# Performance work log

Hardware: AMD Instinct MI355X
Metric: run time of the kernel (lower is better)

Reference implementation:

```python
import jax, jax.numpy as jnp
import numpy as np

B, C, H, W = 2, 256, 64, 64
NUM_HEADS = 4
HEAD_DIM = C // NUM_HEADS
N = H * W


def setup_inputs() -> dict:
    key = jax.random.key(0)
    ks = jax.random.split(key, 10)
    x = jax.random.normal(ks[0], (B, C, H, W), dtype=jnp.float32)
    # mostly-True mask; diagonal forced True so every row has a valid key
    m = jax.random.uniform(ks[1], (B, N, N)) > 0.1
    spatial_mask = m | jnp.eye(N, dtype=bool)[None]
    s = 1.0 / np.sqrt(C)
    wq = jax.random.normal(ks[2], (C, C), dtype=jnp.float32) * s
    bq = jnp.zeros((C,), jnp.float32)
    wk = jax.random.normal(ks[3], (C, C), dtype=jnp.float32) * s
    bk = jnp.zeros((C,), jnp.float32)
    wv = jax.random.normal(ks[4], (C, C), dtype=jnp.float32) * s
    bv = jnp.zeros((C,), jnp.float32)
    # torch zero-inits out_proj; use random weights for a non-trivial baseline
    wo = jax.random.normal(ks[5], (C, C), dtype=jnp.float32) * s
    bo = jnp.zeros((C,), jnp.float32)
    return {"x": x, "spatial_mask": spatial_mask, "wq": wq, "bq": bq,
            "wk": wk, "bk": bk, "wv": wv, "bv": bv, "wo": wo, "bo": bo}


def reference(x, spatial_mask, wq, bq, wk, bk, wv, bv, wo, bo):
    b, c, h, w = x.shape
    n = h * w
    nh, hd = NUM_HEADS, HEAD_DIM
    scale = hd ** -0.5
    x_flat = x.reshape(b, c, n).transpose(0, 2, 1)           # [b, n, c]
    q = (x_flat @ wq.T + bq).reshape(b, n, nh, hd).transpose(0, 2, 1, 3)
    k = (x_flat @ wk.T + bk).reshape(b, n, nh, hd).transpose(0, 2, 1, 3)
    v = (x_flat @ wv.T + bv).reshape(b, n, nh, hd).transpose(0, 2, 1, 3)
    logits = jnp.einsum('bhqd,bhkd->bhqk', q, k) * scale      # [b, nh, n, n]
    logits = jnp.where(spatial_mask[:, None], logits, -jnp.inf)
    attn = jax.nn.softmax(logits, axis=-1)                    # dropout = identity (eval)
    out = jnp.einsum('bhqk,bhkd->bhqd', attn, v)              # [b, nh, n, hd]
    out = out.transpose(0, 2, 1, 3).reshape(b, n, c)
    out = out @ wo.T + bo
    return out.transpose(0, 2, 1).reshape(b, c, h, w)
```

## Files before the change

### kernel.cpp

```cpp
#include <hip/hip_runtime.h>
#include <math.h>

namespace {
constexpr int B_    = 2;
constexpr int C_    = 256;
constexpr int NHEAD = 4;
constexpr int HDIM  = 64;
constexpr int NTOK  = 4096;
constexpr float SCALE = 0.125f;
constexpr float LOG2E = 1.44269504f;
}

typedef _Float16 half8  __attribute__((ext_vector_type(8)));
typedef _Float16 half4  __attribute__((ext_vector_type(4)));
typedef float    floatx4 __attribute__((ext_vector_type(4)));

__global__ __launch_bounds__(256) void pack_mask(
    const unsigned int* __restrict__ m32, unsigned int* __restrict__ packed)
{
    int c0 = 0, c1 = 0, c2 = 0, c3 = 0;
    #pragma unroll
    for (int i = 0; i < 16; i++) {
        const unsigned int d = m32[i];
        c0 += (d == 0x00000001u);
        c1 += (d == 0x3F803F80u);
        c2 += (d == 0x3F800000u);
        c3 += (d == 0x01010101u);
    }
    int fmt = 1, best = c1;
    if (c0 > best) { best = c0; fmt = 0; }
    if (c2 > best) { best = c2; fmt = 2; }
    if (c3 > best) { best = c3; fmt = 3; }

    const unsigned int W = blockIdx.x * 256 + threadIdx.x;
    unsigned int bits = 0;
    if (fmt == 1) {
        const uint4* p4 = (const uint4*)(m32 + (size_t)W * 16);
        #pragma unroll
        for (int i = 0; i < 4; i++) {
            const uint4 v = p4[i];
            const unsigned int d[4] = { v.x, v.y, v.z, v.w };
            #pragma unroll
            for (int j = 0; j < 4; j++) {
                const int e = i * 8 + j * 2;
                bits |= ((d[j] & 0xFFFFu) ? 1u : 0u) << e;
                bits |= ((d[j] >> 16)     ? 1u : 0u) << (e + 1);
            }
        }
    } else if (fmt != 3) {
        const uint4* p4 = (const uint4*)(m32 + (size_t)W * 32);
        #pragma unroll
        for (int i = 0; i < 8; i++) {
            const uint4 v = p4[i];
            bits |= (v.x ? 1u : 0u) << (i * 4 + 0);
            bits |= (v.y ? 1u : 0u) << (i * 4 + 1);
            bits |= (v.z ? 1u : 0u) << (i * 4 + 2);
            bits |= (v.w ? 1u : 0u) << (i * 4 + 3);
        }
    } else {
        const uint4* p4 = (const uint4*)(m32 + (size_t)W * 8);
        #pragma unroll
        for (int i = 0; i < 2; i++) {
            const uint4 v = p4[i];
            const unsigned int d[4] = { v.x, v.y, v.z, v.w };
            #pragma unroll
            for (int j = 0; j < 4; j++) {
                const int e = (i * 4 + j) * 4;
                bits |= ((d[j] & 0x000000FFu) ? 1u : 0u) << (e + 0);
                bits |= ((d[j] & 0x0000FF00u) ? 1u : 0u) << (e + 1);
                bits |= ((d[j] & 0x00FF0000u) ? 1u : 0u) << (e + 2);
                bits |= ((d[j] & 0xFF000000u) ? 1u : 0u) << (e + 3);
            }
        }
    }
    packed[W] = bits;
}

__global__ __launch_bounds__(256) void qkv_mfma(
    const float* __restrict__ x,
    const float* __restrict__ wq, const float* __restrict__ bq,
    const float* __restrict__ wk, const float* __restrict__ bk,
    const float* __restrict__ wv, const float* __restrict__ bv,
    _Float16* __restrict__ qo, _Float16* __restrict__ ko,
    _Float16* __restrict__ vo)
{
    const int nt = blockIdx.x;
    const int h  = blockIdx.y;
    const int b  = blockIdx.z / 3;
    const int p  = blockIdx.z % 3;

    const float* w; const float* bias;
    if (p == 0)      { w = wq; bias = bq; }
    else if (p == 1) { w = wk; bias = bk; }
    else             { w = wv; bias = bv; }

    const int t    = threadIdx.x;
    const int wid  = t >> 6;
    const int lane = t & 63;
    const int quad = lane >> 4;
    const int l15  = lane & 15;
    const int n0  = nt * 64;
    const int co0 = h * 64;

    __shared__ _Float16 wsh[64 * 72];
    __shared__ _Float16 xsh[64 * 72];
    __shared__ _Float16 tbuf[64 * 72];

    const int srow = t >> 2;
    const int sc   = (t & 3) * 16;
    const int cr   = t >> 4;
    const int nu   = (t & 15) * 4;

    floatx4 acc[4];
    #pragma unroll
    for (int i = 0; i < 4; i++) acc[i] = (floatx4)0.f;

    const float* xb = x + (size_t)b * C_ * NTOK;

    for (int c0 = 0; c0 < C_; c0 += 64) {
        {
            const float* wr = &w[(size_t)(co0 + srow) * C_ + c0 + sc];
            half8 h0, h1;
            #pragma unroll
            for (int u = 0; u < 2; u++) {
                const float4 a = *(const float4*)&wr[u * 4];
                h0[u*4+0]=(_Float16)a.x; h0[u*4+1]=(_Float16)a.y;
                h0[u*4+2]=(_Float16)a.z; h0[u*4+3]=(_Float16)a.w;
            }
            #pragma unroll
            for (int u = 0; u < 2; u++) {
                const float4 a = *(const float4*)&wr[8 + u * 4];
                h1[u*4+0]=(_Float16)a.x; h1[u*4+1]=(_Float16)a.y;
                h1[u*4+2]=(_Float16)a.z; h1[u*4+3]=(_Float16)a.w;
            }
            *(half8*)&wsh[srow * 72 + sc]     = h0;
            *(half8*)&wsh[srow * 72 + sc + 8] = h1;
        }
        {
            #pragma unroll
            for (int pass = 0; pass < 4; pass++) {
                const int cl = pass * 16 + cr;
                const float4 v = *(const float4*)&xb[(size_t)(c0 + cl) * NTOK + n0 + nu];
                xsh[(nu + 0) * 72 + cl] = (_Float16)v.x;
                xsh[(nu + 1) * 72 + cl] = (_Float16)v.y;
                xsh[(nu + 2) * 72 + cl] = (_Float16)v.z;
                xsh[(nu + 3) * 72 + cl] = (_Float16)v.w;
            }
        }
        __syncthreads();
        const half8 a0 = *(const half8*)&wsh[(wid * 16 + l15) * 72 + quad * 8];
        const half8 a1 = *(const half8*)&wsh[(wid * 16 + l15) * 72 + 32 + quad * 8];
        #pragma unroll
        for (int nt2 = 0; nt2 < 4; nt2++) {
            const half8 b0 = *(const half8*)&xsh[(nt2 * 16 + l15) * 72 + quad * 8];
            const half8 b1 = *(const half8*)&xsh[(nt2 * 16 + l15) * 72 + 32 + quad * 8];
            acc[nt2] = __builtin_amdgcn_mfma_f32_16x16x32_f16(a0, b0, acc[nt2], 0, 0, 0);
            acc[nt2] = __builtin_amdgcn_mfma_f32_16x16x32_f16(a1, b1, acc[nt2], 0, 0, 0);
        }
        __syncthreads();
    }

    const float4 bb4 = *(const float4*)&bias[co0 + wid * 16 + quad * 4];
    const float bb[4] = { bb4.x, bb4.y, bb4.z, bb4.w };

    if (p < 2) {
        const float osc = (p == 0) ? (SCALE * LOG2E) : 1.0f;
        #pragma unroll
        for (int nt2 = 0; nt2 < 4; nt2++) {
            half4 hv;
            #pragma unroll
            for (int i = 0; i < 4; i++)
                hv[i] = (_Float16)((acc[nt2][i] + bb[i]) * osc);
            *(half4*)&tbuf[(nt2 * 16 + l15) * 72 + wid * 16 + quad * 4] = hv;
        }
        __syncthreads();
        _Float16* dh = (p == 0 ? qo : ko) + (size_t)(b * NHEAD + h) * NTOK * HDIM;
        const half8 o0 = *(const half8*)&tbuf[srow * 72 + sc];
        const half8 o1 = *(const half8*)&tbuf[srow * 72 + sc + 8];
        *(half8*)&dh[(size_t)(n0 + srow) * HDIM + sc]     = o0;
        *(half8*)&dh[(size_t)(n0 + srow) * HDIM + sc + 8] = o1;
    } else {
        #pragma unroll
        for (int nt2 = 0; nt2 < 4; nt2++)
            #pragma unroll
            for (int i = 0; i < 4; i++)
                tbuf[(wid * 16 + quad * 4 + i) * 72 + nt2 * 16 + l15] =
                    (_Float16)(acc[nt2][i] + bb[i]);
        __syncthreads();
        _Float16* vth = vo + (size_t)(b * NHEAD + h) * HDIM * NTOK;
        const half8 o0 = *(const half8*)&tbuf[srow * 72 + sc];
        const half8 o1 = *(const half8*)&tbuf[srow * 72 + sc + 8];
        *(half8*)&vth[(size_t)srow * NTOK + n0 + sc]     = o0;
        *(half8*)&vth[(size_t)srow * NTOK + n0 + sc + 8] = o1;
    }
}

__global__ __launch_bounds__(512) void attn(
    const _Float16* __restrict__ q, const _Float16* __restrict__ k,
    const _Float16* __restrict__ vt, const unsigned int* __restrict__ mpacked,
    _Float16* __restrict__ ao)
{
    const int b  = blockIdx.z;
    const int h  = blockIdx.y;
    const int q0 = blockIdx.x * 64;
    const int t    = threadIdx.x;
    const int w    = t >> 6;
    const int lane = t & 63;
    const int quad = lane >> 4;
    const int l15  = lane & 15;
    const int half = w >> 2;
    const int w4   = w & 3;
    const int koff = half * (NTOK / 2);

    __shared__ __align__(16) _Float16 ksA[64 * 72];
    __shared__ __align__(16) _Float16 vsA[64 * 72];
    __shared__ __align__(16) _Float16 psA[64 * 72];
    __shared__ __align__(16) _Float16 ksB[64 * 72];
    __shared__ __align__(16) _Float16 vsB[64 * 72];
    __shared__ __align__(16) _Float16 psB[64 * 72];

    _Float16* ksc = half ? ksB : ksA;
    _Float16* vsc = half ? vsB : vsA;
    _Float16* ps  = half ? psB : psA;

    const size_t head_off = (size_t)(b * NHEAD + h) * NTOK * HDIM;
    const _Float16* qb  = q  + head_off;
    const _Float16* kb  = k  + head_off;
    const _Float16* vtb = vt + head_off;
    const unsigned int* mrow = mpacked + (size_t)b * NTOK * 128;

    const int qrow = q0 + w4 * 16 + l15;
    half8 aq0 = *(const half8*)&qb[(size_t)qrow * HDIM + quad * 8];
    half8 aq1 = *(const half8*)&qb[(size_t)qrow * HDIM + 32 + quad * 8];
    const unsigned int* mq = &mrow[(size_t)qrow * 128];

    const int tl   = t & 255;
    const int srow = tl >> 2;
    const int scol = (tl & 3) * 16;

    half8 kreg0 = *(const half8*)&kb[(size_t)(koff + srow) * HDIM + scol];
    half8 kreg1 = *(const half8*)&kb[(size_t)(koff + srow) * HDIM + scol + 8];
    half8 vreg0 = *(const half8*)&vtb[(size_t)srow * NTOK + koff + scol];
    half8 vreg1 = *(const half8*)&vtb[(size_t)srow * NTOK + koff + scol + 8];

    float l_loc = 0.f;
    floatx4 o_acc[4];
    #pragma unroll
    for (int i = 0; i < 4; i++) o_acc[i] = (floatx4)0.f;

    for (int kt = 0; kt < NTOK / 128; kt++) {
        const int k0 = koff + kt * 64;
        __syncthreads();
        *(half8*)&ksc[srow * 72 + scol]     = kreg0;
        *(half8*)&ksc[srow * 72 + scol + 8] = kreg1;
        *(half8*)&vsc[srow * 72 + scol]     = vreg0;
        *(half8*)&vsc[srow * 72 + scol + 8] = vreg1;
        __syncthreads();

        if (kt + 1 < NTOK / 128) {
            kreg0 = *(const half8*)&kb[(size_t)(k0 + 64 + srow) * HDIM + scol];
            kreg1 = *(const half8*)&kb[(size_t)(k0 + 64 + srow) * HDIM + scol + 8];
            vreg0 = *(const half8*)&vtb[(size_t)srow * NTOK + k0 + 64 + scol];
            vreg1 = *(const half8*)&vtb[(size_t)srow * NTOK + k0 + 64 + scol + 8];
        }
        const uint2 mw = *(const uint2*)&mq[k0 >> 5];

        floatx4 sa[4];
        #pragma unroll
        for (int ct = 0; ct < 4; ct++) {
            sa[ct] = (floatx4)0.f;
            const half8 ka0 = *(const half8*)&ksc[(ct * 16 + l15) * 72 + quad * 8];
            const half8 ka1 = *(const half8*)&ksc[(ct * 16 + l15) * 72 + 32 + quad * 8];
            sa[ct] = __builtin_amdgcn_mfma_f32_16x16x32_f16(ka0, aq0, sa[ct], 0, 0, 0);
            sa[ct] = __builtin_amdgcn_mfma_f32_16x16x32_f16(ka1, aq1, sa[ct], 0, 0, 0);
        }

        #pragma unroll
        for (int ct = 0; ct < 4; ct++) {
            const unsigned int word = (ct < 2) ? mw.x : mw.y;
            const unsigned nib = (word >> (((ct & 1) << 4) + quad * 4)) & 0xFu;
            half4 pv;
            #pragma unroll
            for (int i = 0; i < 4; i++) {
                const float v = ((nib >> i) & 1u) ? sa[ct][i] : -3.0e38f;
                const float p = exp2f(fminf(v, 15.f));
                l_loc += p;
                pv[i] = (_Float16)p;
            }
            *(half4*)&ps[(w4 * 16 + l15) * 72 + ct * 16 + quad * 4] = pv;
        }

        const half8 pb0 = *(const half8*)&ps[(w4 * 16 + l15) * 72 + quad * 8];
        const half8 pb1 = *(const half8*)&ps[(w4 * 16 + l15) * 72 + 32 + quad * 8];
        #pragma unroll
        for (int dt = 0; dt < 4; dt++) {
            const half8 va0 = *(const half8*)&vsc[(dt * 16 + l15) * 72 + quad * 8];
            const half8 va1 = *(const half8*)&vsc[(dt * 16 + l15) * 72 + 32 + quad * 8];
            o_acc[dt] = __builtin_amdgcn_mfma_f32_16x16x32_f16(va0, pb0, o_acc[dt], 0, 0, 0);
            o_acc[dt] = __builtin_amdgcn_mfma_f32_16x16x32_f16(va1, pb1, o_acc[dt], 0, 0, 0);
        }
    }

    l_loc += __shfl_xor(l_loc, 16, 64);
    l_loc += __shfl_xor(l_loc, 32, 64);

    __syncthreads();
    float* oex = (float*)ksA;
    float* lex = (float*)vsA;
    if (w >= 4) {
        float* dst = &oex[((size_t)(w - 4) * 64 + lane) * 16];
        #pragma unroll
        for (int dt = 0; dt < 4; dt++)
            *(floatx4*)&dst[dt * 4] = o_acc[dt];
        if (quad == 0) lex[(w - 4) * 16 + l15] = l_loc;
    }
    __syncthreads();
    if (w < 4) {
        const float* src = &oex[((size_t)w * 64 + lane) * 16];
        const float lt = l_loc + lex[w * 16 + l15];
        const float inv = (lt > 0.f) ? (1.0f / lt) : 0.f;
        _Float16* aob = ao + ((size_t)b * NTOK + q0 + w * 16 + l15) * C_ + h * 64;
        #pragma unroll
        for (int dt = 0; dt < 4; dt++) {
            const floatx4 o2 = *(const floatx4*)&src[dt * 4];
            half4 r;
            #pragma unroll
            for (int rr = 0; rr < 4; rr++)
                r[rr] = (_Float16)((o_acc[dt][rr] + o2[rr]) * inv);
            *(half4*)&aob[dt * 16 + quad * 4] = r;
        }
    }
}

__global__ __launch_bounds__(256) void out_mfma(
    const _Float16* __restrict__ ao, const float* __restrict__ wo,
    const float* __restrict__ bo, float* __restrict__ out)
{
    const int nt  = blockIdx.x;
    const int cot = blockIdx.y;
    const int b   = blockIdx.z;
    const int t    = threadIdx.x;
    const int wid  = t >> 6;
    const int lane = t & 63;
    const int quad = lane >> 4;
    const int l15  = lane & 15;
    const int n0  = nt * 64;
    const int co0 = cot * 64;

    __shared__ _Float16 wsh[64 * 72];
    __shared__ _Float16 ash[64 * 72];
    __shared__ float    tf[64 * 68];

    const int srow = t >> 2;
    const int sc   = (t & 3) * 16;

    floatx4 acc[4];
    #pragma unroll
    for (int i = 0; i < 4; i++) acc[i] = (floatx4)0.f;

    const _Float16* aob = ao + ((size_t)b * NTOK + n0) * C_;

    for (int c0 = 0; c0 < C_; c0 += 64) {
        {
            const float* wr = &wo[(size_t)(co0 + srow) * C_ + c0 + sc];
            half8 h0, h1;
            #pragma unroll
            for (int u = 0; u < 2; u++) {
                const float4 a = *(const float4*)&wr[u * 4];
                h0[u*4+0]=(_Float16)a.x; h0[u*4+1]=(_Float16)a.y;
                h0[u*4+2]=(_Float16)a.z; h0[u*4+3]=(_Float16)a.w;
            }
            #pragma unroll
            for (int u = 0; u < 2; u++) {
                const float4 a = *(const float4*)&wr[8 + u * 4];
                h1[u*4+0]=(_Float16)a.x; h1[u*4+1]=(_Float16)a.y;
                h1[u*4+2]=(_Float16)a.z; h1[u*4+3]=(_Float16)a.w;
            }
            *(half8*)&wsh[srow * 72 + sc]     = h0;
            *(half8*)&wsh[srow * 72 + sc + 8] = h1;
        }
        {
            const _Float16* ar = &aob[(size_t)srow * C_ + c0 + sc];
            *(half8*)&ash[srow * 72 + sc]     = *(const half8*)&ar[0];
            *(half8*)&ash[srow * 72 + sc + 8] = *(const half8*)&ar[8];
        }
        __syncthreads();
        const half8 a0 = *(const half8*)&wsh[(wid * 16 + l15) * 72 + quad * 8];
        const half8 a1 = *(const half8*)&wsh[(wid * 16 + l15) * 72 + 32 + quad * 8];
        #pragma unroll
        for (int nt2 = 0; nt2 < 4; nt2++) {
            const half8 b0 = *(const half8*)&ash[(nt2 * 16 + l15) * 72 + quad * 8];
            const half8 b1 = *(const half8*)&ash[(nt2 * 16 + l15) * 72 + 32 + quad * 8];
            acc[nt2] = __builtin_amdgcn_mfma_f32_16x16x32_f16(a0, b0, acc[nt2], 0, 0, 0);
            acc[nt2] = __builtin_amdgcn_mfma_f32_16x16x32_f16(a1, b1, acc[nt2], 0, 0, 0);
        }
        __syncthreads();
    }

    #pragma unroll
    for (int nt2 = 0; nt2 < 4; nt2++)
        #pragma unroll
        for (int i = 0; i < 4; i++)
            tf[(wid * 16 + quad * 4 + i) * 68 + nt2 * 16 + l15] = acc[nt2][i];
    __syncthreads();

    const int row = t >> 2;
    const int c4  = (t & 3) * 16;
    const float bb = bo[co0 + row];
    float* orow = &out[((size_t)(b * C_ + co0 + row)) * NTOK + n0 + c4];
    #pragma unroll
    for (int u = 0; u < 4; u++) {
        float4 v = *(const float4*)&tf[row * 68 + c4 + u * 4];
        v.x += bb; v.y += bb; v.z += bb; v.w += bb;
        *(float4*)&orow[u * 4] = v;
    }
}

extern "C" void kernel_launch(void* const* d_in, const int* in_sizes, int n_in,
                              void* d_out, int out_size, void* d_ws, size_t ws_size,
                              hipStream_t stream) {
    const float* x    = (const float*)d_in[0];
    const void*  mask = d_in[1];
    const float* wq   = (const float*)d_in[2];
    const float* bq   = (const float*)d_in[3];
    const float* wk   = (const float*)d_in[4];
    const float* bk   = (const float*)d_in[5];
    const float* wv   = (const float*)d_in[6];
    const float* bv   = (const float*)d_in[7];
    const float* wo   = (const float*)d_in[8];
    const float* bo   = (const float*)d_in[9];
    float* out = (float*)d_out;

    const size_t qkv_elems = (size_t)B_ * NHEAD * NTOK * HDIM;
    _Float16* wsh = (_Float16*)d_ws;
    _Float16* qbuf  = wsh;
    _Float16* kbuf  = wsh + qkv_elems;
    _Float16* vtbuf = wsh + 2 * qkv_elems;
    _Float16* aobuf = wsh + 3 * qkv_elems;
    unsigned int* mpacked = (unsigned int*)(wsh + 4 * qkv_elems);

    pack_mask<<<dim3((B_ * NTOK * 128) / 256), 256, 0, stream>>>(
        (const unsigned int*)mask, mpacked);
    qkv_mfma<<<dim3(NTOK / 64, NHEAD, B_ * 3), 256, 0, stream>>>(
        x, wq, bq, wk, bk, wv, bv, qbuf, kbuf, vtbuf);
    attn<<<dim3(NTOK / 64, NHEAD, B_), 512, 0, stream>>>(
        qbuf, kbuf, vtbuf, mpacked, aobuf);
    out_mfma<<<dim3(NTOK / 64, C_ / 64, B_), 256, 0, stream>>>(
        aobuf, wo, bo, out);
}
```

Measured before the change: 318.3 us.

## Stage full x tile once per block across heads; cheapen softmax exp/convert

The QKV projection kernel now loads and converts the whole 64-token by 256-channel x tile into shared memory once, then loops over all four heads inside the block. This replaces the earlier design of one block per head, which re-read x once per head. The grid shrinks to 4x fewer blocks, which lowers parallelism, and shared memory use per block grows. In the attention kernel, the masked exp2 now uses the hardware builtin without the fminf clamp, and the fp16 conversion uses packed round-toward-zero. That removes some ALU work but drops the overflow guard and changes the rounding mode.

```diff
diff --git a/kernel.cpp b/kernel.cpp
--- a/kernel.cpp
+++ b/kernel.cpp
@@ -13,6 +13,7 @@
 
 typedef _Float16 half8  __attribute__((ext_vector_type(8)));
 typedef _Float16 half4  __attribute__((ext_vector_type(4)));
+typedef __fp16   fp16x2 __attribute__((ext_vector_type(2)));
 typedef float    floatx4 __attribute__((ext_vector_type(4)));
 
 __global__ __launch_bounds__(256) void pack_mask(
@@ -85,9 +86,8 @@
     _Float16* __restrict__ vo)
 {
     const int nt = blockIdx.x;
-    const int h  = blockIdx.y;
-    const int b  = blockIdx.z / 3;
-    const int p  = blockIdx.z % 3;
+    const int b  = blockIdx.y;
+    const int p  = blockIdx.z;
 
     const float* w; const float* bias;
     if (p == 0)      { w = wq; bias = bq; }
@@ -99,99 +99,102 @@
     const int lane = t & 63;
     const int quad = lane >> 4;
     const int l15  = lane & 15;
-    const int n0  = nt * 64;
-    const int co0 = h * 64;
-
+    const int n0   = nt * 64;
+
+    __shared__ _Float16 xsh[64 * 264];
     __shared__ _Float16 wsh[64 * 72];
-    __shared__ _Float16 xsh[64 * 72];
     __shared__ _Float16 tbuf[64 * 72];
 
     const int srow = t >> 2;
     const int sc   = (t & 3) * 16;
-    const int cr   = t >> 4;
-    const int nu   = (t & 15) * 4;
-
-    floatx4 acc[4];
-    #pragma unroll
-    for (int i = 0; i < 4; i++) acc[i] = (floatx4)0.f;
-
-    const float* xb = x + (size_t)b * C_ * NTOK;
-
-    for (int c0 = 0; c0 < C_; c0 += 64) {
-        {
-            const float* wr = &w[(size_t)(co0 + srow) * C_ + c0 + sc];
-            half8 h0, h1;
-            #pragma unroll
-            for (int u = 0; u < 2; u++) {
-                const float4 a = *(const float4*)&wr[u * 4];
-                h0[u*4+0]=(_Float16)a.x; h0[u*4+1]=(_Float16)a.y;
-                h0[u*4+2]=(_Float16)a.z; h0[u*4+3]=(_Float16)a.w;
-            }
-            #pragma unroll
-            for (int u = 0; u < 2; u++) {
-                const float4 a = *(const float4*)&wr[8 + u * 4];
-                h1[u*4+0]=(_Float16)a.x; h1[u*4+1]=(_Float16)a.y;
-                h1[u*4+2]=(_Float16)a.z; h1[u*4+3]=(_Float16)a.w;
-            }
-            *(half8*)&wsh[srow * 72 + sc]     = h0;
-            *(half8*)&wsh[srow * 72 + sc + 8] = h1;
-        }
-        {
-            #pragma unroll
-            for (int pass = 0; pass < 4; pass++) {
-                const int cl = pass * 16 + cr;
-                const float4 v = *(const float4*)&xb[(size_t)(c0 + cl) * NTOK + n0 + nu];
-                xsh[(nu + 0) * 72 + cl] = (_Float16)v.x;
-                xsh[(nu + 1) * 72 + cl] = (_Float16)v.y;
-                xsh[(nu + 2) * 72 + cl] = (_Float16)v.z;
-                xsh[(nu + 3) * 72 + cl] = (_Float16)v.w;
-            }
+
+    {
+        const int cr = t >> 4;
+        const int nu = (t & 15) * 4;
+        const float* xb = x + (size_t)b * C_ * NTOK;
+        #pragma unroll
+        for (int cc = 0; cc < 16; cc++) {
+            const int cl = cc * 16 + cr;
+            const float4 v = *(const float4*)&xb[(size_t)cl * NTOK + n0 + nu];
+            xsh[(nu + 0) * 264 + cl] = (_Float16)v.x;
+            xsh[(nu + 1) * 264 + cl] = (_Float16)v.y;
+            xsh[(nu + 2) * 264 + cl] = (_Float16)v.z;
+            xsh[(nu + 3) * 264 + cl] = (_Float16)v.w;
+        }
+    }
+
+    for (int h = 0; h < NHEAD; h++) {
+        const int co0 = h * 64;
+        floatx4 acc[4];
+        #pragma unroll
+        for (int i = 0; i < 4; i++) acc[i] = (floatx4)0.f;
+
+        for (int c0 = 0; c0 < C_; c0 += 64) {
+            {
+                const float* wr = &w[(size_t)(co0 + srow) * C_ + c0 + sc];
+                half8 h0, h1;
+                #pragma unroll
+                for (int u = 0; u < 2; u++) {
+                    const float4 a = *(const float4*)&wr[u * 4];
+                    h0[u*4+0]=(_Float16)a.x; h0[u*4+1]=(_Float16)a.y;
+                    h0[u*4+2]=(_Float16)a.z; h0[u*4+3]=(_Float16)a.w;
+                }
+                #pragma unroll
+                for (int u = 0; u < 2; u++) {
+                    const float4 a = *(const float4*)&wr[8 + u * 4];
+                    h1[u*4+0]=(_Float16)a.x; h1[u*4+1]=(_Float16)a.y;
+                    h1[u*4+2]=(_Float16)a.z; h1[u*4+3]=(_Float16)a.w;
+                }
+                *(half8*)&wsh[srow * 72 + sc]     = h0;
+                *(half8*)&wsh[srow * 72 + sc + 8] = h1;
+            }
+            __syncthreads();
+            const half8 a0 = *(const half8*)&wsh[(wid * 16 + l15) * 72 + quad * 8];
+            const half8 a1 = *(const half8*)&wsh[(wid * 16 + l15) * 72 + 32 + quad * 8];
+            #pragma unroll
+            for (int nt2 = 0; nt2 < 4; nt2++) {
+                const half8 b0 = *(const half8*)&xsh[(nt2 * 16 + l15) * 264 + c0 + quad * 8];
+                const half8 b1 = *(const half8*)&xsh[(nt2 * 16 + l15) * 264 + c0 + 32 + quad * 8];
+                acc[nt2] = __builtin_amdgcn_mfma_f32_16x16x32_f16(a0, b0, acc[nt2], 0, 0, 0);
+                acc[nt2] = __builtin_amdgcn_mfma_f32_16x16x32_f16(a1, b1, acc[nt2], 0, 0, 0);
+            }
+            __syncthreads();
+        }
+
+        const float4 bb4 = *(const float4*)&bias[co0 + wid * 16 + quad * 4];
+        const float bb[4] = { bb4.x, bb4.y, bb4.z, bb4.w };
+
+        if (p < 2) {
+            const float osc = (p == 0) ? (SCALE * LOG2E) : 1.0f;
+            #pragma unroll
+            for (int nt2 = 0; nt2 < 4; nt2++) {
+                half4 hv;
+                #pragma unroll
+                for (int i = 0; i < 4; i++)
+                    hv[i] = (_Float16)((acc[nt2][i] + bb[i]) * osc);
+                *(half4*)&tbuf[(nt2 * 16 + l15) * 72 + wid * 16 + quad * 4] = hv;
+            }
+            __syncthreads();
+            _Float16* dh = (p == 0 ? qo : ko) + (size_t)(b * NHEAD + h) * NTOK * HDIM;
+            const half8 o0 = *(const half8*)&tbuf[srow * 72 + sc];
+            const half8 o1 = *(const half8*)&tbuf[srow * 72 + sc + 8];
+            *(half8*)&dh[(size_t)(n0 + srow) * HDIM + sc]     = o0;
+            *(half8*)&dh[(size_t)(n0 + srow) * HDIM + sc + 8] = o1;
+        } else {
+            #pragma unroll
+            for (int nt2 = 0; nt2 < 4; nt2++)
+                #pragma unroll
+                for (int i = 0; i < 4; i++)
+                    tbuf[(wid * 16 + quad * 4 + i) * 72 + nt2 * 16 + l15] =
+                        (_Float16)(acc[nt2][i] + bb[i]);
+            __syncthreads();
+            _Float16* vth = vo + (size_t)(b * NHEAD + h) * HDIM * NTOK;
+            const half8 o0 = *(const half8*)&tbuf[srow * 72 + sc];
+            const half8 o1 = *(const half8*)&tbuf[srow * 72 + sc + 8];
+            *(half8*)&vth[(size_t)srow * NTOK + n0 + sc]     = o0;
+            *(half8*)&vth[(size_t)srow * NTOK + n0 + sc + 8] = o1;
         }
         __syncthreads();
-        const half8 a0 = *(const half8*)&wsh[(wid * 16 + l15) * 72 + quad * 8];
-        const half8 a1 = *(const half8*)&wsh[(wid * 16 + l15) * 72 + 32 + quad * 8];
-        #pragma unroll
-        for (int nt2 = 0; nt2 < 4; nt2++) {
-            const half8 b0 = *(const half8*)&xsh[(nt2 * 16 + l15) * 72 + quad * 8];
-            const half8 b1 = *(const half8*)&xsh[(nt2 * 16 + l15) * 72 + 32 + quad * 8];
-            acc[nt2] = __builtin_amdgcn_mfma_f32_16x16x32_f16(a0, b0, acc[nt2], 0, 0, 0);
-            acc[nt2] = __builtin_amdgcn_mfma_f32_16x16x32_f16(a1, b1, acc[nt2], 0, 0, 0);
-        }
-        __syncthreads();
-    }
-
-    const float4 bb4 = *(const float4*)&bias[co0 + wid * 16 + quad * 4];
-    const float bb[4] = { bb4.x, bb4.y, bb4.z, bb4.w };
-
-    if (p < 2) {
-        const float osc = (p == 0) ? (SCALE * LOG2E) : 1.0f;
-        #pragma unroll
-        for (int nt2 = 0; nt2 < 4; nt2++) {
-            half4 hv;
-            #pragma unroll
-            for (int i = 0; i < 4; i++)
-                hv[i] = (_Float16)((acc[nt2][i] + bb[i]) * osc);
-            *(half4*)&tbuf[(nt2 * 16 + l15) * 72 + wid * 16 + quad * 4] = hv;
-        }
-        __syncthreads();
-        _Float16* dh = (p == 0 ? qo : ko) + (size_t)(b * NHEAD + h) * NTOK * HDIM;
-        const half8 o0 = *(const half8*)&tbuf[srow * 72 + sc];
-        const half8 o1 = *(const half8*)&tbuf[srow * 72 + sc + 8];
-        *(half8*)&dh[(size_t)(n0 + srow) * HDIM + sc]     = o0;
-        *(half8*)&dh[(size_t)(n0 + srow) * HDIM + sc + 8] = o1;
-    } else {
-        #pragma unroll
-        for (int nt2 = 0; nt2 < 4; nt2++)
-            #pragma unroll
-            for (int i = 0; i < 4; i++)
-                tbuf[(wid * 16 + quad * 4 + i) * 72 + nt2 * 16 + l15] =
-                    (_Float16)(acc[nt2][i] + bb[i]);
-        __syncthreads();
-        _Float16* vth = vo + (size_t)(b * NHEAD + h) * HDIM * NTOK;
-        const half8 o0 = *(const half8*)&tbuf[srow * 72 + sc];
-        const half8 o1 = *(const half8*)&tbuf[srow * 72 + sc + 8];
-        *(half8*)&vth[(size_t)srow * NTOK + n0 + sc]     = o0;
-        *(half8*)&vth[(size_t)srow * NTOK + n0 + sc + 8] = o1;
     }
 }
 
@@ -248,6 +251,8 @@
     #pragma unroll
     for (int i = 0; i < 4; i++) o_acc[i] = (floatx4)0.f;
 
+    _Float16* psrow = &ps[(w4 * 16 + l15) * 72];
+
     for (int kt = 0; kt < NTOK / 128; kt++) {
         const int k0 = koff + kt * 64;
         __syncthreads();
@@ -279,19 +284,21 @@
         for (int ct = 0; ct < 4; ct++) {
             const unsigned int word = (ct < 2) ? mw.x : mw.y;
             const unsigned nib = (word >> (((ct & 1) << 4) + quad * 4)) & 0xFu;
+            const float p0 = __builtin_amdgcn_exp2f((nib & 1u) ? sa[ct][0] : -3.0e38f);
+            const float p1 = __builtin_amdgcn_exp2f((nib & 2u) ? sa[ct][1] : -3.0e38f);
+            const float p2 = __builtin_amdgcn_exp2f((nib & 4u) ? sa[ct][2] : -3.0e38f);
+            const float p3 = __builtin_amdgcn_exp2f((nib & 8u) ? sa[ct][3] : -3.0e38f);
+            l_loc += (p0 + p1) + (p2 + p3);
+            const fp16x2 lo = __builtin_amdgcn_cvt_pkrtz(p0, p1);
+            const fp16x2 hi = __builtin_amdgcn_cvt_pkrtz(p2, p3);
             half4 pv;
-            #pragma unroll
-            for (int i = 0; i < 4; i++) {
-                const float v = ((nib >> i) & 1u) ? sa[ct][i] : -3.0e38f;
-                const float p = exp2f(fminf(v, 15.f));
-                l_loc += p;
-                pv[i] = (_Float16)p;
-            }
-            *(half4*)&ps[(w4 * 16 + l15) * 72 + ct * 16 + quad * 4] = pv;
-        }
-
-        const half8 pb0 = *(const half8*)&ps[(w4 * 16 + l15) * 72 + quad * 8];
-        const half8 pb1 = *(const half8*)&ps[(w4 * 16 + l15) * 72 + 32 + quad * 8];
+            pv[0] = (_Float16)lo[0]; pv[1] = (_Float16)lo[1];
+            pv[2] = (_Float16)hi[0]; pv[3] = (_Float16)hi[1];
+            *(half4*)&psrow[ct * 16 + quad * 4] = pv;
+        }
+
+        const half8 pb0 = *(const half8*)&psrow[quad * 8];
+        const half8 pb1 = *(const half8*)&psrow[32 + quad * 8];
         #pragma unroll
         for (int dt = 0; dt < 4; dt++) {
             const half8 va0 = *(const half8*)&vsc[(dt * 16 + l15) * 72 + quad * 8];
@@ -441,7 +448,7 @@
 
     pack_mask<<<dim3((B_ * NTOK * 128) / 256), 256, 0, stream>>>(
         (const unsigned int*)mask, mpacked);
-    qkv_mfma<<<dim3(NTOK / 64, NHEAD, B_ * 3), 256, 0, stream>>>(
+    qkv_mfma<<<dim3(NTOK / 64, B_, 3), 256, 0, stream>>>(
         x, wq, bq, wk, bk, wv, bv, qbuf, kbuf, vtbuf);
     attn<<<dim3(NTOK / 64, NHEAD, B_), 512, 0, stream>>>(
         qbuf, kbuf, vtbuf, mpacked, aobuf);
```

New measurement: 309.3 us. 2.8% less time.
